# Performance work log

Hardware: AMD Instinct MI355X
Metric: run time of the kernel (lower is better)

## Reference

```python
import jax, jax.numpy as jnp
import numpy as np

B, H, W, C = 4, 48, 48, 256
NUM_HEADS = 8
DEPTH = C // NUM_HEADS  # 32


def setup_inputs() -> dict:
    key = jax.random.key(0)
    ks = jax.random.split(key, 8)
    scale = 1.0 / np.sqrt(C)
    return {
        "inputs": jax.random.normal(ks[0], (B, H, W, C), dtype=jnp.float32),
        "wq": jax.random.normal(ks[1], (C, C), dtype=jnp.float32) * scale,
        "bq": jax.random.normal(ks[2], (C,), dtype=jnp.float32) * 0.01,
        "wk": jax.random.normal(ks[3], (C, C), dtype=jnp.float32) * scale,
        "bk": jax.random.normal(ks[4], (C,), dtype=jnp.float32) * 0.01,
        "wv": jax.random.normal(ks[5], (C, C), dtype=jnp.float32) * scale,
        "bv": jax.random.normal(ks[6], (C,), dtype=jnp.float32) * 0.01,
        "gamma": jax.random.normal(ks[7], (), dtype=jnp.float32) * 0.1,
    }


def reference(inputs, wq, bq, wk, bk, wv, bv, gamma):
    b, h, w, c = inputs.shape
    n = h * w  # number of tokens

    def proj_split(wm, bm):
        # 1x1 conv == per-pixel dense: [b,h,w,c] @ [c,c] + bias
        y = jnp.einsum('bhwc,cd->bhwd', inputs, wm) + bm
        # split heads -> [b, num_heads, n, depth]
        return y.reshape(b, n, NUM_HEADS, DEPTH).transpose(0, 2, 1, 3)

    q = proj_split(wq, bq) / jnp.sqrt(jnp.asarray(DEPTH, inputs.dtype))
    k = proj_split(wk, bk)
    v = proj_split(wv, bv)

    s = jnp.einsum('bnqd,bnkd->bnqk', q, k)        # [b, heads, n, n]
    a = jax.nn.softmax(s, axis=-1)
    o = jnp.einsum('bnqk,bnkd->bnqd', a, v)        # [b, heads, n, depth]
    o = o.transpose(0, 2, 1, 3).reshape(b, h, w, c)
    return gamma * o + inputs
```

## Files before the change

### kernel.cpp

```cpp
#include <hip/hip_runtime.h>
#include <hip/hip_bf16.h>
#include <cstdint>

#define B_    4
#define NH    8
#define N_TOK 2304
#define D_    32
#define C_    256
#define M_ROWS (B_ * N_TOK)
#define KVB   128
#define NT2   (N_TOK / KVB)
#define M_FIX 10.0f

typedef float  f32x4  __attribute__((ext_vector_type(4)));
typedef short  bf16x8 __attribute__((ext_vector_type(8)));

#define GLOADLDS(g, l) __builtin_amdgcn_global_load_lds( \
    (const __attribute__((address_space(1))) unsigned*)(g), \
    (__attribute__((address_space(3))) unsigned*)(l), 16, 0, 0)

static __device__ __forceinline__ unsigned short f2bf(float f) {
    union { float f; unsigned u; } v; v.f = f;
    unsigned u = v.u;
    u += 0x7FFF + ((u >> 16) & 1);
    return (unsigned short)(u >> 16);
}

static __device__ __forceinline__ unsigned cvt_pk_bf16(float a, float b) {
    unsigned r;
    asm("v_cvt_pk_bf16_f32 %0, %1, %2" : "=v"(r) : "v"(a), "v"(b));
    return r;
}

__global__ void k_prep_x(const float* __restrict__ x, unsigned short* __restrict__ xb) {
    int i = blockIdx.x * blockDim.x + threadIdx.x;
    float4 v = reinterpret_cast<const float4*>(x)[i];
    ushort4 o;
    o.x = f2bf(v.x); o.y = f2bf(v.y); o.z = f2bf(v.z); o.w = f2bf(v.w);
    reinterpret_cast<ushort4*>(xb)[i] = o;
}

__global__ void k_prep_w(const float* __restrict__ w0, const float* __restrict__ w1,
                         const float* __restrict__ w2, unsigned short* __restrict__ wt) {
    __shared__ float tile[64][65];
    int mat = blockIdx.y;
    const float* w = (mat == 0) ? w0 : (mat == 1) ? w1 : w2;
    int t   = blockIdx.x;
    int tc  = (t & 3) * 64;
    int td  = (t >> 2) * 64;
    int tid = threadIdx.x;
    int r0  = tid >> 6;
    int x0  = tid & 63;
#pragma unroll
    for (int it = 0; it < 16; ++it) {
        int c = it * 4 + r0;
        tile[c][x0] = w[(tc + c) * C_ + td + x0];
    }
    __syncthreads();
    unsigned short* wto = wt + mat * (C_ * C_);
#pragma unroll
    for (int it = 0; it < 16; ++it) {
        int d = it * 4 + r0;
        wto[(td + d) * C_ + tc + x0] = f2bf(tile[x0][d]);
    }
}

__global__ __launch_bounds__(256) void k_proj(
    const unsigned short* __restrict__ xb,
    const unsigned short* __restrict__ wtb,
    const float* __restrict__ bq, const float* __restrict__ bk, const float* __restrict__ bv,
    unsigned short* __restrict__ qo, unsigned short* __restrict__ ko, unsigned short* __restrict__ vto)
{
    __shared__ __align__(16) unsigned short A_lds[3][64][32];
    __shared__ __align__(16) unsigned short B_lds[3][128][32];

    int rows0 = blockIdx.x * 64;
    int cols0 = blockIdx.y * 128;
    int mat   = cols0 >> 8;
    const float* bias = (mat == 0) ? bq : (mat == 1) ? bk : bv;
    float scale = (mat == 0) ? (0.17677669529663687f * 1.4426950408889634f) : 1.0f;

    int tid = threadIdx.x, wave = tid >> 6, lane = tid & 63;
    int lr = lane & 15, lg = lane >> 4;
    int wr = wave >> 1, wc = wave & 1;

    int srow = lane >> 2, sslot = lane & 3;
    int ra   = wave * 16 + srow;
    int keyA = ((ra >> 1) & 1) | (((ra >> 3) & 1) << 1);
    const unsigned short* asrc = xb + (rows0 + ra) * C_ + ((sslot ^ keyA) * 8);
    int rb   = wave * 32 + srow;
    int keyB0 = ((rb >> 1) & 1) | (((rb >> 3) & 1) << 1);
    int keyB1 = (((rb + 16) >> 1) & 1) | ((((rb + 16) >> 3) & 1) << 1);
    const unsigned short* bsrc0 = wtb + (cols0 + rb) * C_ + ((sslot ^ keyB0) * 8);
    const unsigned short* bsrc1 = wtb + (cols0 + rb + 16) * C_ + ((sslot ^ keyB1) * 8);

    char* aldsb = (char*)&A_lds[0][0][0];
    char* bldsb = (char*)&B_lds[0][0][0];
    int adst = wave * 1024;
    int bdst0 = wave * 2048, bdst1 = bdst0 + 1024;

    int xorb = (((lr >> 1) & 1) << 4) | (((lr >> 3) & 1) << 5);
    int fcol = (lg * 16) ^ xorb;
    int arow0 = wr * 32 + lr;
    int brow0 = wc * 64 + lr;

#define PSTAGE(ks, bidx) do {                               \
        int ko_ = (ks) * 32;                                \
        char* ad = aldsb + (bidx) * 4096;                   \
        char* bd = bldsb + (bidx) * 8192;                   \
        GLOADLDS(asrc + ko_, ad + adst);                    \
        GLOADLDS(bsrc0 + ko_, bd + bdst0);                  \
        GLOADLDS(bsrc1 + ko_, bd + bdst1);                  \
    } while (0)

    PSTAGE(0, 0);
    PSTAGE(1, 1);
    asm volatile("s_waitcnt vmcnt(3)" ::: "memory");
    __builtin_amdgcn_s_barrier();

    f32x4 acc[2][4];
#pragma unroll
    for (int i = 0; i < 2; ++i)
#pragma unroll
        for (int j = 0; j < 4; ++j) acc[i][j] = (f32x4){0.f, 0.f, 0.f, 0.f};

    int b0 = 0;
    for (int ks = 0; ks < 8; ++ks) {
        if (ks + 2 < 8) {
            int b2 = b0 + 2; if (b2 >= 3) b2 -= 3;
            PSTAGE(ks + 2, b2);
        }
        const char* ac = aldsb + b0 * 4096;
        const char* bc = bldsb + b0 * 8192;

        bf16x8 a[2], b[4];
#pragma unroll
        for (int fr = 0; fr < 2; ++fr)
            a[fr] = *reinterpret_cast<const bf16x8*>(ac + (arow0 + fr * 16) * 64 + fcol);
#pragma unroll
        for (int fn = 0; fn < 4; ++fn)
            b[fn] = *reinterpret_cast<const bf16x8*>(bc + (brow0 + fn * 16) * 64 + fcol);

        __builtin_amdgcn_s_setprio(1);
#pragma unroll
        for (int fr = 0; fr < 2; ++fr)
#pragma unroll
            for (int fn = 0; fn < 4; ++fn)
                acc[fr][fn] = __builtin_amdgcn_mfma_f32_16x16x32_bf16(a[fr], b[fn], acc[fr][fn], 0, 0, 0);
        __builtin_amdgcn_s_setprio(0);

        if (ks < 7) {
            if (ks + 2 < 8) asm volatile("s_waitcnt vmcnt(3)" ::: "memory");
            else            asm volatile("s_waitcnt vmcnt(0)" ::: "memory");
            __builtin_amdgcn_s_barrier();
        }
        b0 = (b0 + 1 == 3) ? 0 : b0 + 1;
    }
#undef PSTAGE

    int bidx = rows0 / N_TOK;
    int nb   = rows0 - bidx * N_TOK + wr * 32 + lg * 4;

    if (mat == 2) {
#pragma unroll
        for (int fr = 0; fr < 2; ++fr)
#pragma unroll
            for (int fn = 0; fn < 4; ++fn) {
                int cm = (cols0 & 255) + wc * 64 + fn * 16 + lr;
                float bsv = bias[cm];
                int hh = cm >> 5, d = cm & 31;
                uint2 pr;
                pr.x = cvt_pk_bf16(acc[fr][fn][0] + bsv, acc[fr][fn][1] + bsv);
                pr.y = cvt_pk_bf16(acc[fr][fn][2] + bsv, acc[fr][fn][3] + bsv);
                *reinterpret_cast<uint2*>(vto + ((bidx * NH + hh) * D_ + d) * N_TOK + nb + fr * 16) = pr;
            }
    } else {
        unsigned short* dst = (mat == 0) ? qo : ko;
#pragma unroll
        for (int fr = 0; fr < 2; ++fr)
#pragma unroll
            for (int fn = 0; fn < 4; ++fn) {
                int cm = (cols0 & 255) + wc * 64 + fn * 16 + lr;
                float bsv = bias[cm];
                int hh = cm >> 5, d = cm & 31;
#pragma unroll
                for (int j = 0; j < 4; ++j) {
                    float val = (acc[fr][fn][j] + bsv) * scale;
                    dst[((bidx * NH + hh) * N_TOK + nb + fr * 16 + j) * D_ + d] = f2bf(val);
                }
            }
    }
}

__global__ __launch_bounds__(256, 3) void k_attn(
    const unsigned short* __restrict__ qb,
    const unsigned short* __restrict__ kb,
    const unsigned short* __restrict__ vtg,
    const float* __restrict__ x,
    const float* __restrict__ gamma_p,
    float* __restrict__ out)
{
    __shared__ __align__(16) unsigned short K_lds[3][KVB][32];
    __shared__ __align__(16) unsigned short Vt_lds[3][32][KVB];

    int wid = (blockIdx.x & 7) * 72 + (blockIdx.x >> 3);
    int bh  = wid / 18;
    int qb0 = (wid % 18) * 128;

    int tid = threadIdx.x, wave = tid >> 6, lane = tid & 63;
    int lr = lane & 15, lg = lane >> 4;

    const unsigned short* Q  = qb  + bh * N_TOK * D_;
    const unsigned short* K  = kb  + bh * N_TOK * D_;
    const unsigned short* Vt = vtg + bh * D_ * N_TOK;

    int qrowA = qb0 + wave * 32 + lr;
    bf16x8 qA = *reinterpret_cast<const bf16x8*>(Q + qrowA * D_ + lg * 8);
    bf16x8 qB = *reinterpret_cast<const bf16x8*>(Q + (qrowA + 16) * D_ + lg * 8);

    bool stK  = wave < 2;
    int cbase = (stK ? wave : (wave - 2)) * 4;
    int r = lane >> 2, sslot = lane & 3;
    int kslot = ((r >> 1) & 1) | (((r >> 3) & 1) << 1);
    int c8 = lane & 15;
    int off0, off1, off2, off3;
    if (stK) {
        off0 = (16 * (cbase + 0) + r) * D_ + ((sslot ^ kslot) * 8);
        off1 = (16 * (cbase + 1) + r) * D_ + ((sslot ^ kslot) * 8);
        off2 = (16 * (cbase + 2) + r) * D_ + ((sslot ^ kslot) * 8);
        off3 = (16 * (cbase + 3) + r) * D_ + ((sslot ^ kslot) * 8);
    } else {
        int r0 = 4 * (cbase + 0) + (lane >> 4);
        int r1 = 4 * (cbase + 1) + (lane >> 4);
        int r2 = 4 * (cbase + 2) + (lane >> 4);
        int r3 = 4 * (cbase + 3) + (lane >> 4);
        off0 = r0 * N_TOK + ((c8 ^ (r0 & 7)) * 8);
        off1 = r1 * N_TOK + ((c8 ^ (r1 & 7)) * 8);
        off2 = r2 * N_TOK + ((c8 ^ (r2 & 7)) * 8);
        off3 = r3 * N_TOK + ((c8 ^ (r3 & 7)) * 8);
    }
    int dstA = (cbase + 0) * 1024 + lane * 16;
    int dstB = dstA + 1024, dstC = dstA + 2048, dstD = dstA + 3072;

    const unsigned short* sbase = stK ? K : Vt;
    int stp = stK ? (KVB * D_) : KVB;
    char* lbase = stK ? (char*)&K_lds[0][0][0] : (char*)&Vt_lds[0][0][0];
    char* kldsb = (char*)&K_lds[0][0][0];
    char* vldsb = (char*)&Vt_lds[0][0][0];

#define STAGE(st, bidx) do {                                \
        const unsigned short* sp = sbase + (st) * stp;      \
        char* ld = lbase + (bidx) * 8192;                   \
        GLOADLDS(sp + off0, ld + dstA);                     \
        GLOADLDS(sp + off1, ld + dstB);                     \
        GLOADLDS(sp + off2, ld + dstC);                     \
        GLOADLDS(sp + off3, ld + dstD);                     \
    } while (0)

    STAGE(0, 0);
    STAGE(1, 1);
    asm volatile("s_waitcnt vmcnt(4)" ::: "memory");
    __builtin_amdgcn_s_barrier();

    f32x4 accA0 = (f32x4){0.f, 0.f, 0.f, 0.f};
    f32x4 accA1 = (f32x4){0.f, 0.f, 0.f, 0.f};
    f32x4 accB0 = (f32x4){0.f, 0.f, 0.f, 0.f};
    f32x4 accB1 = (f32x4){0.f, 0.f, 0.f, 0.f};
    f32x4 acclA = (f32x4){0.f, 0.f, 0.f, 0.f};
    f32x4 acclB = (f32x4){0.f, 0.f, 0.f, 0.f};

    union { unsigned w[4]; bf16x8 v; } ones;
    ones.w[0] = 0x3F803F80u; ones.w[1] = 0x3F803F80u;
    ones.w[2] = 0x3F803F80u; ones.w[3] = 0x3F803F80u;

    int kread_key = (((lr >> 1) & 1) << 4) | (((lr >> 2) & 1) << 5);
    int krow_lane = (8 * (lr >> 2) + (lr & 3)) * 64 + ((lg * 16) ^ kread_key);
    int vkey = (lr & 7) << 4;

    const f32x4 zinit = (f32x4){-M_FIX, -M_FIX, -M_FIX, -M_FIX};

    int b0 = 0;
    for (int t = 0; t < NT2; ++t) {
        if (t + 2 < NT2) {
            int b2 = b0 + 2; if (b2 >= 3) b2 -= 3;
            STAGE(t + 2, b2);
        }
        const char* kc = kldsb + b0 * 8192;
        const char* vc = vldsb + b0 * 8192;

        f32x4 sA[8], sB[8];
        __builtin_amdgcn_s_setprio(1);
#pragma unroll
        for (int kt = 0; kt < 8; ++kt) {
            bf16x8 kf = *reinterpret_cast<const bf16x8*>(
                kc + (kt >> 1) * 2048 + (kt & 1) * 256 + krow_lane);
            sA[kt] = __builtin_amdgcn_mfma_f32_16x16x32_bf16(kf, qA, zinit, 0, 0, 0);
            sB[kt] = __builtin_amdgcn_mfma_f32_16x16x32_bf16(kf, qB, zinit, 0, 0, 0);
        }
        __builtin_amdgcn_s_setprio(0);

#pragma unroll
        for (int kseg = 0; kseg < 4; ++kseg) {
            union { unsigned w[4]; bf16x8 v; } paA, paB;
            paA.w[0] = cvt_pk_bf16(__builtin_amdgcn_exp2f(sA[2 * kseg][0]),
                                   __builtin_amdgcn_exp2f(sA[2 * kseg][1]));
            paA.w[1] = cvt_pk_bf16(__builtin_amdgcn_exp2f(sA[2 * kseg][2]),
                                   __builtin_amdgcn_exp2f(sA[2 * kseg][3]));
            paA.w[2] = cvt_pk_bf16(__builtin_amdgcn_exp2f(sA[2 * kseg + 1][0]),
                                   __builtin_amdgcn_exp2f(sA[2 * kseg + 1][1]));
            paA.w[3] = cvt_pk_bf16(__builtin_amdgcn_exp2f(sA[2 * kseg + 1][2]),
                                   __builtin_amdgcn_exp2f(sA[2 * kseg + 1][3]));
            paB.w[0] = cvt_pk_bf16(__builtin_amdgcn_exp2f(sB[2 * kseg][0]),
                                   __builtin_amdgcn_exp2f(sB[2 * kseg][1]));
            paB.w[1] = cvt_pk_bf16(__builtin_amdgcn_exp2f(sB[2 * kseg][2]),
                                   __builtin_amdgcn_exp2f(sB[2 * kseg][3]));
            paB.w[2] = cvt_pk_bf16(__builtin_amdgcn_exp2f(sB[2 * kseg + 1][0]),
                                   __builtin_amdgcn_exp2f(sB[2 * kseg + 1][1]));
            paB.w[3] = cvt_pk_bf16(__builtin_amdgcn_exp2f(sB[2 * kseg + 1][2]),
                                   __builtin_amdgcn_exp2f(sB[2 * kseg + 1][3]));
            int off = (kseg * 64 + lg * 16) ^ vkey;
            bf16x8 vf0 = *reinterpret_cast<const bf16x8*>(vc + lr * 256 + off);
            bf16x8 vf1 = *reinterpret_cast<const bf16x8*>(vc + (16 + lr) * 256 + off);
            accA0 = __builtin_amdgcn_mfma_f32_16x16x32_bf16(paA.v, vf0,    accA0, 0, 0, 0);
            accA1 = __builtin_amdgcn_mfma_f32_16x16x32_bf16(paA.v, vf1,    accA1, 0, 0, 0);
            accB0 = __builtin_amdgcn_mfma_f32_16x16x32_bf16(paB.v, vf0,    accB0, 0, 0, 0);
            accB1 = __builtin_amdgcn_mfma_f32_16x16x32_bf16(paB.v, vf1,    accB1, 0, 0, 0);
            acclA = __builtin_amdgcn_mfma_f32_16x16x32_bf16(paA.v, ones.v, acclA, 0, 0, 0);
            acclB = __builtin_amdgcn_mfma_f32_16x16x32_bf16(paB.v, ones.v, acclB, 0, 0, 0);
        }

        if (t < NT2 - 1) {
            if (t + 2 < NT2) asm volatile("s_waitcnt vmcnt(4)" ::: "memory");
            else             asm volatile("s_waitcnt vmcnt(0)" ::: "memory");
            __builtin_amdgcn_s_barrier();
        }
        b0 = (b0 + 1 == 3) ? 0 : b0 + 1;
    }
#undef STAGE

    float g = gamma_p[0];
    int b = bh >> 3, head = bh & 7;
#pragma unroll
    for (int j = 0; j < 4; ++j) {
        float linvA = 1.0f / acclA[j];
        float linvB = 1.0f / acclB[j];
        int nA = qb0 + wave * 32 + 4 * lg + j;
        long rA = (long)(b * N_TOK + nA) * C_ + head * 32;
        long rB = rA + 16L * C_;
        out[rA + lr]      = g * (accA0[j] * linvA) + x[rA + lr];
        out[rA + 16 + lr] = g * (accA1[j] * linvA) + x[rA + 16 + lr];
        out[rB + lr]      = g * (accB0[j] * linvB) + x[rB + lr];
        out[rB + 16 + lr] = g * (accB1[j] * linvB) + x[rB + 16 + lr];
    }
}

extern "C" void kernel_launch(void* const* d_in, const int* in_sizes, int n_in,
                              void* d_out, int out_size, void* d_ws, size_t ws_size,
                              hipStream_t stream) {
    const float* x     = (const float*)d_in[0];
    const float* wq    = (const float*)d_in[1];
    const float* bq    = (const float*)d_in[2];
    const float* wk    = (const float*)d_in[3];
    const float* bk    = (const float*)d_in[4];
    const float* wv    = (const float*)d_in[5];
    const float* bv    = (const float*)d_in[6];
    const float* gamma = (const float*)d_in[7];
    float* out = (float*)d_out;

    char* ws = (char*)d_ws;
    unsigned short* xb   = (unsigned short*)(ws);
    unsigned short* wt   = (unsigned short*)(ws + 4718592);
    unsigned short* qbuf = (unsigned short*)(ws + 5111808);
    unsigned short* kbuf = (unsigned short*)(ws + 9830400);
    unsigned short* vtg  = (unsigned short*)(ws + 14548992);

    k_prep_x<<<dim3(M_ROWS * C_ / 1024), dim3(256), 0, stream>>>(x, xb);
    k_prep_w<<<dim3(16, 3), dim3(256), 0, stream>>>(wq, wk, wv, wt);
    k_proj<<<dim3(M_ROWS / 64, 6), dim3(256), 0, stream>>>(xb, wt, bq, bk, bv, qbuf, kbuf, vtg);
    k_attn<<<dim3(N_TOK / 128 * B_ * NH), dim3(256), 0, stream>>>(qbuf, kbuf, vtg, x, gamma, out);
}
```

Measured before the change: 60.66 us.

## Halve attention KV tile and merge prep kernels into one launch

Shrinks the key/value tile streamed through LDS from 128 to 64 tokens and rewrites the staging address math to match, cutting LDS use and score registers so the launch bound can rise to four blocks per CU. It also folds the x-to-bf16 conversion and the weight transpose into a single kernel to save one launch. The smaller tile doubles the number of loop iterations and barriers per block and leaves less work to hide each load behind.

```diff
diff --git a/kernel.cpp b/kernel.cpp
--- a/kernel.cpp
+++ b/kernel.cpp
@@ -8,7 +8,7 @@
 #define D_    32
 #define C_    256
 #define M_ROWS (B_ * N_TOK)
-#define KVB   128
+#define KVB   64
 #define NT2   (N_TOK / KVB)
 #define M_FIX 10.0f
 
@@ -32,20 +32,23 @@
     return r;
 }
 
-__global__ void k_prep_x(const float* __restrict__ x, unsigned short* __restrict__ xb) {
-    int i = blockIdx.x * blockDim.x + threadIdx.x;
-    float4 v = reinterpret_cast<const float4*>(x)[i];
-    ushort4 o;
-    o.x = f2bf(v.x); o.y = f2bf(v.y); o.z = f2bf(v.z); o.w = f2bf(v.w);
-    reinterpret_cast<ushort4*>(xb)[i] = o;
-}
-
-__global__ void k_prep_w(const float* __restrict__ w0, const float* __restrict__ w1,
-                         const float* __restrict__ w2, unsigned short* __restrict__ wt) {
+__global__ void k_prep(const float* __restrict__ x,
+                       const float* __restrict__ w0, const float* __restrict__ w1,
+                       const float* __restrict__ w2,
+                       unsigned short* __restrict__ xb, unsigned short* __restrict__ wt) {
     __shared__ float tile[64][65];
-    int mat = blockIdx.y;
+    int bid = blockIdx.x;
+    if (bid < 2304) {
+        int i = bid * 256 + threadIdx.x;
+        float4 v = reinterpret_cast<const float4*>(x)[i];
+        ushort4 o;
+        o.x = f2bf(v.x); o.y = f2bf(v.y); o.z = f2bf(v.z); o.w = f2bf(v.w);
+        reinterpret_cast<ushort4*>(xb)[i] = o;
+        return;
+    }
+    int t   = bid - 2304;
+    int mat = t >> 4;  t &= 15;
     const float* w = (mat == 0) ? w0 : (mat == 1) ? w1 : w2;
-    int t   = blockIdx.x;
     int tc  = (t & 3) * 64;
     int td  = (t >> 2) * 64;
     int tid = threadIdx.x;
@@ -192,7 +195,7 @@
     }
 }
 
-__global__ __launch_bounds__(256, 3) void k_attn(
+__global__ __launch_bounds__(256, 4) void k_attn(
     const unsigned short* __restrict__ qb,
     const unsigned short* __restrict__ kb,
     const unsigned short* __restrict__ vtg,
@@ -218,48 +221,40 @@
     bf16x8 qA = *reinterpret_cast<const bf16x8*>(Q + qrowA * D_ + lg * 8);
     bf16x8 qB = *reinterpret_cast<const bf16x8*>(Q + (qrowA + 16) * D_ + lg * 8);
 
-    bool stK  = wave < 2;
-    int cbase = (stK ? wave : (wave - 2)) * 4;
-    int r = lane >> 2, sslot = lane & 3;
-    int kslot = ((r >> 1) & 1) | (((r >> 3) & 1) << 1);
-    int c8 = lane & 15;
-    int off0, off1, off2, off3;
-    if (stK) {
-        off0 = (16 * (cbase + 0) + r) * D_ + ((sslot ^ kslot) * 8);
-        off1 = (16 * (cbase + 1) + r) * D_ + ((sslot ^ kslot) * 8);
-        off2 = (16 * (cbase + 2) + r) * D_ + ((sslot ^ kslot) * 8);
-        off3 = (16 * (cbase + 3) + r) * D_ + ((sslot ^ kslot) * 8);
-    } else {
-        int r0 = 4 * (cbase + 0) + (lane >> 4);
-        int r1 = 4 * (cbase + 1) + (lane >> 4);
-        int r2 = 4 * (cbase + 2) + (lane >> 4);
-        int r3 = 4 * (cbase + 3) + (lane >> 4);
-        off0 = r0 * N_TOK + ((c8 ^ (r0 & 7)) * 8);
-        off1 = r1 * N_TOK + ((c8 ^ (r1 & 7)) * 8);
-        off2 = r2 * N_TOK + ((c8 ^ (r2 & 7)) * 8);
-        off3 = r3 * N_TOK + ((c8 ^ (r3 & 7)) * 8);
-    }
-    int dstA = (cbase + 0) * 1024 + lane * 16;
-    int dstB = dstA + 1024, dstC = dstA + 2048, dstD = dstA + 3072;
-
-    const unsigned short* sbase = stK ? K : Vt;
-    int stp = stK ? (KVB * D_) : KVB;
-    char* lbase = stK ? (char*)&K_lds[0][0][0] : (char*)&Vt_lds[0][0][0];
+    bool stK = wave < 2;
+    int kr0   = 32 * wave + (lane >> 2);
+    int kslot = ((kr0 >> 1) & 1) | (((kr0 >> 3) & 1) << 1);
+    int koff0 = kr0 * D_ + (((lane & 3) ^ kslot) * 8);
+    int koff1 = koff0 + 16 * D_;
+    int kdst0 = wave * 2048 + lane * 16;
+    int kdst1 = kdst0 + 1024;
+    int vw    = wave - 2;
+    int vr0   = 16 * vw + (lane >> 3);
+    int vkeyw = vr0 & 7;
+    int voff0 = vr0 * N_TOK + (((lane & 7) ^ vkeyw) * 8);
+    int voff1 = (vr0 + 8) * N_TOK + (((lane & 7) ^ vkeyw) * 8);
+    int vdst0 = vw * 2048 + lane * 16;
+    int vdst1 = vdst0 + 1024;
+
     char* kldsb = (char*)&K_lds[0][0][0];
     char* vldsb = (char*)&Vt_lds[0][0][0];
 
-#define STAGE(st, bidx) do {                                \
-        const unsigned short* sp = sbase + (st) * stp;      \
-        char* ld = lbase + (bidx) * 8192;                   \
-        GLOADLDS(sp + off0, ld + dstA);                     \
-        GLOADLDS(sp + off1, ld + dstB);                     \
-        GLOADLDS(sp + off2, ld + dstC);                     \
-        GLOADLDS(sp + off3, ld + dstD);                     \
-    } while (0)
+#define STAGE(st, bidx) do {                                    \
+        if (stK) {                                              \
+            const unsigned short* Kn = K + (st) * (KVB * D_);   \
+            char* kd = kldsb + (bidx) * 4096;                   \
+            GLOADLDS(Kn + koff0, kd + kdst0);                   \
+            GLOADLDS(Kn + koff1, kd + kdst1);                   \
+        } else {                                                \
+            const unsigned short* Vn = Vt + (st) * KVB;         \
+            char* vd = vldsb + (bidx) * 4096;                   \
+            GLOADLDS(Vn + voff0, vd + vdst0);                   \
+            GLOADLDS(Vn + voff1, vd + vdst1);                   \
+        } } while (0)
 
     STAGE(0, 0);
     STAGE(1, 1);
-    asm volatile("s_waitcnt vmcnt(4)" ::: "memory");
+    asm volatile("s_waitcnt vmcnt(2)" ::: "memory");
     __builtin_amdgcn_s_barrier();
 
     f32x4 accA0 = (f32x4){0.f, 0.f, 0.f, 0.f};
@@ -285,13 +280,13 @@
             int b2 = b0 + 2; if (b2 >= 3) b2 -= 3;
             STAGE(t + 2, b2);
         }
-        const char* kc = kldsb + b0 * 8192;
-        const char* vc = vldsb + b0 * 8192;
-
-        f32x4 sA[8], sB[8];
+        const char* kc = kldsb + b0 * 4096;
+        const char* vc = vldsb + b0 * 4096;
+
+        f32x4 sA[4], sB[4];
         __builtin_amdgcn_s_setprio(1);
 #pragma unroll
-        for (int kt = 0; kt < 8; ++kt) {
+        for (int kt = 0; kt < 4; ++kt) {
             bf16x8 kf = *reinterpret_cast<const bf16x8*>(
                 kc + (kt >> 1) * 2048 + (kt & 1) * 256 + krow_lane);
             sA[kt] = __builtin_amdgcn_mfma_f32_16x16x32_bf16(kf, qA, zinit, 0, 0, 0);
@@ -300,7 +295,7 @@
         __builtin_amdgcn_s_setprio(0);
 
 #pragma unroll
-        for (int kseg = 0; kseg < 4; ++kseg) {
+        for (int kseg = 0; kseg < 2; ++kseg) {
             union { unsigned w[4]; bf16x8 v; } paA, paB;
             paA.w[0] = cvt_pk_bf16(__builtin_amdgcn_exp2f(sA[2 * kseg][0]),
                                    __builtin_amdgcn_exp2f(sA[2 * kseg][1]));
@@ -319,8 +314,8 @@
             paB.w[3] = cvt_pk_bf16(__builtin_amdgcn_exp2f(sB[2 * kseg + 1][2]),
                                    __builtin_amdgcn_exp2f(sB[2 * kseg + 1][3]));
             int off = (kseg * 64 + lg * 16) ^ vkey;
-            bf16x8 vf0 = *reinterpret_cast<const bf16x8*>(vc + lr * 256 + off);
-            bf16x8 vf1 = *reinterpret_cast<const bf16x8*>(vc + (16 + lr) * 256 + off);
+            bf16x8 vf0 = *reinterpret_cast<const bf16x8*>(vc + lr * 128 + off);
+            bf16x8 vf1 = *reinterpret_cast<const bf16x8*>(vc + (16 + lr) * 128 + off);
             accA0 = __builtin_amdgcn_mfma_f32_16x16x32_bf16(paA.v, vf0,    accA0, 0, 0, 0);
             accA1 = __builtin_amdgcn_mfma_f32_16x16x32_bf16(paA.v, vf1,    accA1, 0, 0, 0);
             accB0 = __builtin_amdgcn_mfma_f32_16x16x32_bf16(paB.v, vf0,    accB0, 0, 0, 0);
@@ -330,7 +325,7 @@
         }
 
         if (t < NT2 - 1) {
-            if (t + 2 < NT2) asm volatile("s_waitcnt vmcnt(4)" ::: "memory");
+            if (t + 2 < NT2) asm volatile("s_waitcnt vmcnt(2)" ::: "memory");
             else             asm volatile("s_waitcnt vmcnt(0)" ::: "memory");
             __builtin_amdgcn_s_barrier();
         }
@@ -374,8 +369,7 @@
     unsigned short* kbuf = (unsigned short*)(ws + 9830400);
     unsigned short* vtg  = (unsigned short*)(ws + 14548992);
 
-    k_prep_x<<<dim3(M_ROWS * C_ / 1024), dim3(256), 0, stream>>>(x, xb);
-    k_prep_w<<<dim3(16, 3), dim3(256), 0, stream>>>(wq, wk, wv, wt);
+    k_prep<<<dim3(2352), dim3(256), 0, stream>>>(x, wq, wk, wv, xb, wt);
     k_proj<<<dim3(M_ROWS / 64, 6), dim3(256), 0, stream>>>(xb, wt, bq, bk, bv, qbuf, kbuf, vtg);
     k_attn<<<dim3(N_TOK / 128 * B_ * NH), dim3(256), 0, stream>>>(qbuf, kbuf, vtg, x, gamma, out);
 }
```

New measurement: 58.50 us, median of 2. 1.04x faster.
